# Kernel optimization log

Measured on AMD Instinct MI355X. Metric: run time of the kernel, lower is better.

Reference implementation:

```python
import jax, jax.numpy as jnp
import numpy as np

B, N, DI, DS, DP, DM, S = 64, 4096, 64, 64, 64, 128, 7
NUM_ITER = 3
EPS_ATTN = 1e-8
LN_EPS = 1e-5


def setup_inputs() -> dict:
    key = jax.random.key(0)
    ks = jax.random.split(key, 12)
    rn = lambda k, shp, sc=1.0: (jax.random.normal(k, shp, jnp.float32) * sc)
    return {
        "x": rn(ks[0], (B, N, DI)),
        "ln_inp_g": jnp.ones((DI,), jnp.float32),
        "ln_inp_b": jnp.zeros((DI,), jnp.float32),
        "ln_slot_g": jnp.ones((DS,), jnp.float32),
        "ln_slot_b": jnp.zeros((DS,), jnp.float32),
        "slots_init": rn(ks[1], (1, S, DS)),
        "Wk": rn(ks[2], (DI, DP), 1.0 / np.sqrt(DI)),
        "Wv": rn(ks[3], (DI, DP), 1.0 / np.sqrt(DI)),
        "Wq": rn(ks[4], (DS, DP), 1.0 / np.sqrt(DS)),
        "gru_wih": rn(ks[5], (3 * DS, DP), 1.0 / np.sqrt(DS)),
        "gru_whh": rn(ks[6], (3 * DS, DS), 1.0 / np.sqrt(DS)),
        "gru_bih": jnp.zeros((3 * DS,), jnp.float32),
        "gru_bhh": jnp.zeros((3 * DS,), jnp.float32),
        "mlp_w1": rn(ks[7], (DS, DM), 1.0 / np.sqrt(DS)),
        "mlp_b1": jnp.zeros((DM,), jnp.float32),
        "mlp_w2": rn(ks[8], (DM, DS), 1.0 / np.sqrt(DM)),
        "mlp_b2": jnp.zeros((DS,), jnp.float32),
    }


def _layernorm(x, g, b):
    m = jnp.mean(x, axis=-1, keepdims=True)
    v = jnp.mean(jnp.square(x - m), axis=-1, keepdims=True)
    return (x - m) * jax.lax.rsqrt(v + LN_EPS) * g + b


def _gru_cell(u, h, wih, whh, bih, bhh):
    # PyTorch GRUCell semantics
    gi = u @ wih.T + bih  # [*, 3*DS]
    gh = h @ whh.T + bhh
    ir, iz, inn = jnp.split(gi, 3, axis=-1)
    hr, hz, hn = jnp.split(gh, 3, axis=-1)
    r = jax.nn.sigmoid(ir + hr)
    z = jax.nn.sigmoid(iz + hz)
    n = jnp.tanh(inn + r * hn)
    return (1.0 - z) * n + z * h


def reference(x, ln_inp_g, ln_inp_b, ln_slot_g, ln_slot_b, slots_init,
              Wk, Wv, Wq, gru_wih, gru_whh, gru_bih, gru_bhh,
              mlp_w1, mlp_b1, mlp_w2, mlp_b2):
    x = _layernorm(x, ln_inp_g, ln_inp_b)          # [B,N,DI]
    k = x @ Wk                                      # [B,N,DP] (hoisted; x fixed across iters)
    v = x @ Wv                                      # [B,N,DP]
    slots = jnp.broadcast_to(slots_init, (x.shape[0], S, DS))
    scale = 1.0 / np.sqrt(DP)
    for _ in range(NUM_ITER):
        slots_prev = slots
        sn = _layernorm(slots, ln_slot_g, ln_slot_b)
        q = sn @ Wq                                 # [B,S,DP]
        attn = jnp.einsum('bnd,bsd->bns', k, q) * scale
        attn = jax.nn.softmax(attn, axis=-1) + EPS_ATTN      # softmax over slots
        weights = attn / jnp.sum(attn, axis=1, keepdims=True)  # normalize over N
        updates = jnp.einsum('bns,bnd->bsd', weights, v)     # [B,S,DP]
        h = _gru_cell(updates.reshape(-1, DP), slots_prev.reshape(-1, DS),
                      gru_wih, gru_whh, gru_bih, gru_bhh)
        slots = h.reshape(-1, S, DS)
        slots = slots + (jax.nn.relu(slots @ mlp_w1 + mlp_b1) @ mlp_w2 + mlp_b2)
    return slots
```

## Files before the change

### kernel.cpp

```cpp
#include <hip/hip_runtime.h>
#include <stdint.h>

#define L2E 1.44269504088896f

static __device__ __forceinline__ float wsum(float v) {
    #pragma unroll
    for (int m = 1; m < 64; m <<= 1) v += __shfl_xor(v, m, 64);
    return v;
}
static __device__ __forceinline__ float sigm(float x) {
    return 1.0f / (1.0f + __builtin_amdgcn_exp2f(-x * L2E));
}
static __device__ __forceinline__ float tanh_(float x) {
    const float ax = fabsf(x);
    const float t = __builtin_amdgcn_exp2f(-2.0f * ax * L2E);
    const float r = (1.0f - t) / (1.0f + t);
    return (x < 0.f) ? -r : r;
}

__global__ __launch_bounds__(256) void init_kernel(
    const float* __restrict__ s0,
    const float* __restrict__ lsg, const float* __restrict__ lsb,
    const float* __restrict__ Wq,  const float* __restrict__ Wk,
    const float* __restrict__ lig, const float* __restrict__ lib,
    const float* __restrict__ wih, const float* __restrict__ whh,
    float* __restrict__ slots, float* __restrict__ gkq, float* __restrict__ aux,
    float* __restrict__ wihT, float* __restrict__ whhT, float* __restrict__ WkT)
{
    __shared__ float wkT[4096];
    __shared__ float scr[4][64];
    const int tid = threadIdx.x, lane = tid & 63, wv = tid >> 6;
    const int idx = blockIdx.x * 256 + tid;

    if (idx < 12288) {
        const int i = idx / 192, j = idx - i * 192;
        wihT[idx] = wih[j * 64 + i];
    } else if (idx < 24576) {
        const int o = idx - 12288;
        const int i = o / 192, j = o - i * 192;
        whhT[o] = whh[j * 64 + i];
    } else {
        const int o = idx - 24576;
        const int p = o >> 6, d = o & 63;
        WkT[o] = Wk[d * 64 + p];
    }

    const int r = blockIdx.x * 4 + wv;
    const int s = r % 7;
    #pragma unroll
    for (int i = tid; i < 4096; i += 256) {
        const int d = i >> 6, p = i & 63;
        wkT[p * 64 + d] = Wk[i];
    }
    const float h = s0[s * 64 + lane];
    slots[r * 64 + lane] = h;
    __syncthreads();

    const float mean = wsum(h) * (1.0f / 64.0f);
    const float d = h - mean;
    const float var = wsum(d * d) * (1.0f / 64.0f);
    const float rs = rsqrtf(var + 1e-5f);
    const float sn = d * rs * lsg[lane] + lsb[lane];
    scr[wv][lane] = sn;
    __syncthreads();
    float q = 0.f;
    #pragma unroll 8
    for (int i = 0; i < 64; ++i) q = fmaf(scr[wv][i], Wq[i * 64 + lane], q);
    q *= 0.125f;
    __syncthreads();
    scr[wv][lane] = q;
    __syncthreads();
    float kq = 0.f;
    #pragma unroll 8
    for (int p = 0; p < 64; ++p) kq = fmaf(wkT[p * 64 + lane], scr[wv][p], kq);
    const float bk = wsum(lib[lane] * kq);
    const float gk = lig[lane] * kq;
    const float g1 = wsum(gk);
    gkq[r * 64 + lane] = gk;
    if (lane == 0) { aux[r * 2] = g1; aux[r * 2 + 1] = bk; }
}

__global__ __launch_bounds__(256) void attn_kernel(
    const float* __restrict__ x,
    const float* __restrict__ gkq, const float* __restrict__ aux,
    float* __restrict__ Ypart)
{
    __shared__ float xsh[4][32 * 65];
    __shared__ float wsh[4][32][8];
    __shared__ float gkql[448];
    __shared__ float auxl[14];
    __shared__ float ybuf[4][456];
    const int tid = threadIdx.x, lane = tid & 63, wv = tid >> 6;
    const int b = blockIdx.x >> 4, chunk = blockIdx.x & 15;

    gkql[tid] = gkq[b * 448 + tid];
    if (tid < 192) gkql[tid + 256] = gkq[b * 448 + tid + 256];
    if (tid < 14) auxl[tid] = aux[b * 14 + tid];
    __syncthreads();

    const int q5 = lane & 31, h = lane >> 5;
    float Yr[14];
    #pragma unroll
    for (int i = 0; i < 14; ++i) Yr[i] = 0.f;
    float cacc[7] = {0.f, 0.f, 0.f, 0.f, 0.f, 0.f, 0.f};

    const float* tbase = x + (((long)b * 4096) + chunk * 256 + wv * 64) * 64;
    #pragma unroll 1
    for (int pass = 0; pass < 2; ++pass) {
        const float4* src = (const float4*)(tbase + pass * 2048);
        #pragma unroll
        for (int st = 0; st < 8; ++st) {
            const float4 d4 = src[st * 64 + lane];
            const int f = (st * 64 + lane) * 4;
            const int row = f >> 6, dim = f & 63;
            float* dst = &xsh[wv][row * 65 + dim];
            dst[0] = d4.x; dst[1] = d4.y; dst[2] = d4.z; dst[3] = d4.w;
        }

        float xf[32];
        float sum = 0.f, ss = 0.f;
        const float* xr = &xsh[wv][q5 * 65 + h * 32];
        #pragma unroll
        for (int c = 0; c < 32; ++c) {
            xf[c] = xr[c];
            sum += xf[c];
            ss = fmaf(xf[c], xf[c], ss);
        }
        float acc[7];
        #pragma unroll
        for (int s = 0; s < 7; ++s) {
            float a = 0.f;
            const float* gk = &gkql[s * 64 + h * 32];
            #pragma unroll
            for (int c = 0; c < 32; ++c) a = fmaf(xf[c], gk[c], a);
            acc[s] = a;
        }
        sum += __shfl_xor(sum, 32, 64);
        ss  += __shfl_xor(ss, 32, 64);
        #pragma unroll
        for (int s = 0; s < 7; ++s) acc[s] += __shfl_xor(acc[s], 32, 64);

        const float m   = sum * (1.0f / 64.0f);
        const float var = ss * (1.0f / 64.0f) - m * m;
        const float rs  = rsqrtf(var + 1e-5f);
        const float rsm = rs * m;
        float t[7];
        #pragma unroll
        for (int s = 0; s < 7; ++s)
            t[s] = fmaf(rs, acc[s], fmaf(-rsm, auxl[2 * s], auxl[2 * s + 1]));
        float mx = t[0];
        #pragma unroll
        for (int s = 1; s < 7; ++s) mx = fmaxf(mx, t[s]);
        float e[7], se = 0.f;
        #pragma unroll
        for (int s = 0; s < 7; ++s) {
            e[s] = __builtin_amdgcn_exp2f((t[s] - mx) * L2E);
            se += e[s];
        }
        const float inv = 1.0f / se;
        #pragma unroll
        for (int s = 0; s < 7; ++s) {
            const float w = fmaf(e[s], inv, 1e-8f);
            cacc[s] += w;
            if (h == 0) wsh[wv][q5][s] = w * rs;
        }
        if (h == 0) wsh[wv][q5][7] = 0.f;

        #pragma unroll 4
        for (int r2 = 0; r2 < 16; ++r2) {
            const int rr = r2 * 2 + h;
            const float4 p0 = *(const float4*)&wsh[wv][rr][0];
            const float4 p1 = *(const float4*)&wsh[wv][rr][4];
            const float v0 = xsh[wv][rr * 65 + q5 * 2];
            const float v1 = xsh[wv][rr * 65 + q5 * 2 + 1];
            const float ps[7] = {p0.x, p0.y, p0.z, p0.w, p1.x, p1.y, p1.z};
            #pragma unroll
            for (int s = 0; s < 7; ++s) {
                Yr[2 * s]     = fmaf(ps[s], v0, Yr[2 * s]);
                Yr[2 * s + 1] = fmaf(ps[s], v1, Yr[2 * s + 1]);
            }
        }
    }

    #pragma unroll
    for (int i = 0; i < 14; ++i) Yr[i] += __shfl_xor(Yr[i], 32, 64);
    if (h == 0) {
        #pragma unroll
        for (int s = 0; s < 7; ++s) {
            ybuf[wv][s * 64 + q5 * 2]     = Yr[2 * s];
            ybuf[wv][s * 64 + q5 * 2 + 1] = Yr[2 * s + 1];
        }
    }
    #pragma unroll
    for (int s = 0; s < 7; ++s) {
        const float Cs = wsum(cacc[s]) * 0.5f;
        if (lane == 0) ybuf[wv][448 + s] = Cs;
    }
    if (lane == 1) ybuf[wv][455] = 0.f;
    __syncthreads();
    for (int i = tid; i < 455; i += 256)
        Ypart[((long)b * 16 + chunk) * 456 + i] =
            ybuf[0][i] + ybuf[1][i] + ybuf[2][i] + ybuf[3][i];
}

__global__ __launch_bounds__(256) void update_kernel(
    const float* __restrict__ Ypart, float* __restrict__ slots,
    const float* __restrict__ Wv,
    const float* __restrict__ wihT, const float* __restrict__ whhT,
    const float* __restrict__ bih,  const float* __restrict__ bhh,
    const float* __restrict__ w1,   const float* __restrict__ b1,
    const float* __restrict__ w2,   const float* __restrict__ b2,
    const float* __restrict__ lsg,  const float* __restrict__ lsb,
    const float* __restrict__ Wq,   const float* __restrict__ WkT,
    const float* __restrict__ lig,  const float* __restrict__ lib,
    float* __restrict__ gkq, float* __restrict__ aux,
    float* __restrict__ out, int last)
{
    __shared__ float red[4][64];
    __shared__ float c16[16];
    __shared__ float ash[64];
    __shared__ float ush[64];
    __shared__ float hsh[64];
    __shared__ float gish[192], ghsh[192];
    __shared__ float hnsh[64];
    __shared__ float mbsh[128];
    __shared__ float qsh[64];
    const int tid = threadIdx.x, lane = tid & 63, wv = tid >> 6;
    const int r = blockIdx.x;
    const int b = r / 7, s = r - b * 7;
    const float* Yb = Ypart + (long)b * 16 * 456;

    float yp = 0.f;
    #pragma unroll
    for (int c = 0; c < 4; ++c)
        yp += Yb[(wv * 4 + c) * 456 + s * 64 + lane];
    red[wv][lane] = yp;
    if (tid < 16) c16[tid] = Yb[tid * 456 + 448 + s];
    if (tid >= 64 && tid < 128) hsh[tid - 64] = slots[r * 64 + (tid - 64)];
    __syncthreads();

    if (tid < 64) {
        const float Yd = red[0][lane] + red[1][lane] + red[2][lane] + red[3][lane];
        float C = 0.f;
        #pragma unroll
        for (int c = 0; c < 16; ++c) C += c16[c];
        const float Z = wsum(Yd) * (1.0f / 64.0f);
        ash[lane] = (lig[lane] * (Yd - Z) + lib[lane] * C) / C;
    }
    __syncthreads();

    float up = 0.f;
    #pragma unroll
    for (int i = 0; i < 16; ++i) {
        const int ii = wv * 16 + i;
        up = fmaf(ash[ii], Wv[ii * 64 + lane], up);
    }
    red[wv][lane] = up;
    __syncthreads();
    if (tid < 64) ush[lane] = red[0][lane] + red[1][lane] + red[2][lane] + red[3][lane];
    __syncthreads();

    if (tid < 192) {
        float a1 = bih[tid], a2 = bhh[tid];
        #pragma unroll 8
        for (int i = 0; i < 64; ++i) {
            a1 = fmaf(ush[i], wihT[i * 192 + tid], a1);
            a2 = fmaf(hsh[i], whhT[i * 192 + tid], a2);
        }
        gish[tid] = a1; ghsh[tid] = a2;
    }
    __syncthreads();
    if (tid < 64) {
        const float rr = sigm(gish[tid] + ghsh[tid]);
        const float zz = sigm(gish[64 + tid] + ghsh[64 + tid]);
        const float nn = tanh_(gish[128 + tid] + rr * ghsh[128 + tid]);
        hnsh[tid] = (1.f - zz) * nn + zz * hsh[tid];
    }
    __syncthreads();

    if (tid < 128) {
        float m = b1[tid];
        #pragma unroll 8
        for (int i = 0; i < 64; ++i) m = fmaf(hnsh[i], w1[i * 128 + tid], m);
        mbsh[tid] = fmaxf(m, 0.f);
    }
    __syncthreads();

    if (tid < 64) {
        float o = b2[tid];
        #pragma unroll 8
        for (int t = 0; t < 128; ++t) o = fmaf(mbsh[t], w2[t * 64 + tid], o);
        const float snv = hnsh[tid] + o;
        slots[r * 64 + tid] = snv;
        if (last) {
            out[r * 64 + tid] = snv;
        } else {
            const float mean = wsum(snv) * (1.0f / 64.0f);
            const float d = snv - mean;
            const float var = wsum(d * d) * (1.0f / 64.0f);
            const float rs = rsqrtf(var + 1e-5f);
            const float sn = d * rs * lsg[tid] + lsb[tid];
            ash[tid] = sn;
            float q = 0.f;
            #pragma unroll 8
            for (int i = 0; i < 64; ++i) q = fmaf(ash[i], Wq[i * 64 + tid], q);
            qsh[tid] = q * 0.125f;
            float kq = 0.f;
            #pragma unroll 8
            for (int p = 0; p < 64; ++p) kq = fmaf(WkT[p * 64 + tid], qsh[p], kq);
            const float bk = wsum(lib[tid] * kq);
            const float gk = lig[tid] * kq;
            const float g1 = wsum(gk);
            gkq[r * 64 + tid] = gk;
            if (tid == 0) { aux[r * 2] = g1; aux[r * 2 + 1] = bk; }
        }
    }
}

extern "C" void kernel_launch(void* const* d_in, const int* in_sizes, int n_in,
                              void* d_out, int out_size, void* d_ws, size_t ws_size,
                              hipStream_t stream)
{
    const float* x   = (const float*)d_in[0];
    const float* lig = (const float*)d_in[1];
    const float* lib = (const float*)d_in[2];
    const float* lsg = (const float*)d_in[3];
    const float* lsb = (const float*)d_in[4];
    const float* s0  = (const float*)d_in[5];
    const float* Wk  = (const float*)d_in[6];
    const float* Wv  = (const float*)d_in[7];
    const float* Wq  = (const float*)d_in[8];
    const float* wih = (const float*)d_in[9];
    const float* whh = (const float*)d_in[10];
    const float* bih = (const float*)d_in[11];
    const float* bhh = (const float*)d_in[12];
    const float* w1  = (const float*)d_in[13];
    const float* b1  = (const float*)d_in[14];
    const float* w2  = (const float*)d_in[15];
    const float* b2  = (const float*)d_in[16];

    float* f = (float*)d_ws;
    float* gkq   = f; f += 448 * 64;
    float* aux   = f; f += 448 * 2;
    float* slots = f; f += 448 * 64;
    float* Ypart = f; f += (long)64 * 16 * 456;
    float* wihT  = f; f += 64 * 192;
    float* whhT  = f; f += 64 * 192;
    float* WkT   = f; f += 64 * 64;

    init_kernel<<<112, 256, 0, stream>>>(s0, lsg, lsb, Wq, Wk, lig, lib,
                                         wih, whh, slots, gkq, aux,
                                         wihT, whhT, WkT);
    for (int it = 0; it < 3; ++it) {
        attn_kernel<<<1024, 256, 0, stream>>>(x, gkq, aux, Ypart);
        update_kernel<<<448, 256, 0, stream>>>(
            Ypart, slots, Wv, wihT, whhT, bih, bhh, w1, b1, w2, b2,
            lsg, lsb, Wq, WkT, lig, lib, gkq, aux,
            (float*)d_out, it == 2);
    }
}
```

Measured before the change: 235.9 us.

## Restructure attention kernel to register-resident rows with DPP reductions

Rewrites the attention kernel so each 8-lane group owns one row of x, with each lane holding 8 dims in registers. Row stats and dot products are reduced with DPP row operations instead of LDS staging and cross-half shuffles. The weighted-value accumulation is done directly in registers, and the next rows are prefetched one step ahead. This removes the LDS transpose buffers and most LDS traffic, at the cost of heavy register use (56 accumulators plus 56 gk values) and a final 16-way LDS reduction.

```diff
diff --git a/kernel.cpp b/kernel.cpp
--- a/kernel.cpp
+++ b/kernel.cpp
@@ -16,6 +16,18 @@
     const float t = __builtin_amdgcn_exp2f(-2.0f * ax * L2E);
     const float r = (1.0f - t) / (1.0f + t);
     return (x < 0.f) ? -r : r;
+}
+
+template <int CTRL>
+static __device__ __forceinline__ float dppterm(float v) {
+    return __int_as_float(__builtin_amdgcn_update_dpp(
+        0, __float_as_int(v), CTRL, 0xF, 0xF, true));
+}
+static __device__ __forceinline__ float red8(float v) {
+    v += dppterm<0xB1>(v);
+    v += dppterm<0x4E>(v);
+    v += dppterm<0x141>(v);
+    return v;
 }
 
 __global__ __launch_bounds__(256) void init_kernel(
@@ -80,65 +92,65 @@
     if (lane == 0) { aux[r * 2] = g1; aux[r * 2 + 1] = bk; }
 }
 
-__global__ __launch_bounds__(256) void attn_kernel(
+__global__ __launch_bounds__(256, 2) void attn_kernel(
     const float* __restrict__ x,
     const float* __restrict__ gkq, const float* __restrict__ aux,
     float* __restrict__ Ypart)
 {
-    __shared__ float xsh[4][32 * 65];
-    __shared__ float wsh[4][32][8];
-    __shared__ float gkql[448];
-    __shared__ float auxl[14];
-    __shared__ float ybuf[4][456];
+    __shared__ float ybuf[16][460];
     const int tid = threadIdx.x, lane = tid & 63, wv = tid >> 6;
-    const int b = blockIdx.x >> 4, chunk = blockIdx.x & 15;
-
-    gkql[tid] = gkq[b * 448 + tid];
-    if (tid < 192) gkql[tid + 256] = gkq[b * 448 + tid + 256];
-    if (tid < 14) auxl[tid] = aux[b * 14 + tid];
-    __syncthreads();
-
-    const int q5 = lane & 31, h = lane >> 5;
-    float Yr[14];
-    #pragma unroll
-    for (int i = 0; i < 14; ++i) Yr[i] = 0.f;
+    const int b = blockIdx.x >> 4, chunk16 = blockIdx.x & 15;
+    const int ck  = lane & 7;
+    const int rsl = lane >> 3;
+
+    float gk[7][8];
+    {
+        const float4* gp = (const float4*)(gkq + b * 448 + ck * 8);
+        #pragma unroll
+        for (int s = 0; s < 7; ++s) {
+            const float4 u0 = gp[s * 16], u1 = gp[s * 16 + 1];
+            gk[s][0] = u0.x; gk[s][1] = u0.y; gk[s][2] = u0.z; gk[s][3] = u0.w;
+            gk[s][4] = u1.x; gk[s][5] = u1.y; gk[s][6] = u1.z; gk[s][7] = u1.w;
+        }
+    }
+    const float* ab = aux + b * 14;
+    float g1[7], bk[7];
+    #pragma unroll
+    for (int s = 0; s < 7; ++s) { g1[s] = ab[2 * s]; bk[s] = ab[2 * s + 1]; }
+
+    float Yacc[7][8];
+    #pragma unroll
+    for (int s = 0; s < 7; ++s)
+        #pragma unroll
+        for (int j = 0; j < 8; ++j) Yacc[s][j] = 0.f;
     float cacc[7] = {0.f, 0.f, 0.f, 0.f, 0.f, 0.f, 0.f};
 
-    const float* tbase = x + (((long)b * 4096) + chunk * 256 + wv * 64) * 64;
+    const float* rb = x + (((long)b * 4096) + chunk16 * 256 + wv * 64 + rsl) * 64
+                        + ck * 8;
+    float4 a0 = *(const float4*)(rb);
+    float4 a1 = *(const float4*)(rb + 4);
     #pragma unroll 1
-    for (int pass = 0; pass < 2; ++pass) {
-        const float4* src = (const float4*)(tbase + pass * 2048);
-        #pragma unroll
-        for (int st = 0; st < 8; ++st) {
-            const float4 d4 = src[st * 64 + lane];
-            const int f = (st * 64 + lane) * 4;
-            const int row = f >> 6, dim = f & 63;
-            float* dst = &xsh[wv][row * 65 + dim];
-            dst[0] = d4.x; dst[1] = d4.y; dst[2] = d4.z; dst[3] = d4.w;
-        }
-
-        float xf[32];
+    for (int g = 0; g < 8; ++g) {
+        const int gn = (g < 7) ? g + 1 : 7;
+        const float4 b0 = *(const float4*)(rb + gn * 512);
+        const float4 b1 = *(const float4*)(rb + gn * 512 + 4);
+
+        const float xv[8] = {a0.x, a0.y, a0.z, a0.w, a1.x, a1.y, a1.z, a1.w};
         float sum = 0.f, ss = 0.f;
-        const float* xr = &xsh[wv][q5 * 65 + h * 32];
-        #pragma unroll
-        for (int c = 0; c < 32; ++c) {
-            xf[c] = xr[c];
-            sum += xf[c];
-            ss = fmaf(xf[c], xf[c], ss);
-        }
+        #pragma unroll
+        for (int j = 0; j < 8; ++j) { sum += xv[j]; ss = fmaf(xv[j], xv[j], ss); }
         float acc[7];
         #pragma unroll
         for (int s = 0; s < 7; ++s) {
             float a = 0.f;
-            const float* gk = &gkql[s * 64 + h * 32];
             #pragma unroll
-            for (int c = 0; c < 32; ++c) a = fmaf(xf[c], gk[c], a);
+            for (int j = 0; j < 8; ++j) a = fmaf(xv[j], gk[s][j], a);
             acc[s] = a;
         }
-        sum += __shfl_xor(sum, 32, 64);
-        ss  += __shfl_xor(ss, 32, 64);
-        #pragma unroll
-        for (int s = 0; s < 7; ++s) acc[s] += __shfl_xor(acc[s], 32, 64);
+        sum = red8(sum);
+        ss  = red8(ss);
+        #pragma unroll
+        for (int s = 0; s < 7; ++s) acc[s] = red8(acc[s]);
 
         const float m   = sum * (1.0f / 64.0f);
         const float var = ss * (1.0f / 64.0f) - m * m;
@@ -147,7 +159,7 @@
         float t[7];
         #pragma unroll
         for (int s = 0; s < 7; ++s)
-            t[s] = fmaf(rs, acc[s], fmaf(-rsm, auxl[2 * s], auxl[2 * s + 1]));
+            t[s] = fmaf(rs, acc[s], fmaf(-rsm, g1[s], bk[s]));
         float mx = t[0];
         #pragma unroll
         for (int s = 1; s < 7; ++s) mx = fmaxf(mx, t[s]);
@@ -162,45 +174,42 @@
         for (int s = 0; s < 7; ++s) {
             const float w = fmaf(e[s], inv, 1e-8f);
             cacc[s] += w;
-            if (h == 0) wsh[wv][q5][s] = w * rs;
-        }
-        if (h == 0) wsh[wv][q5][7] = 0.f;
-
-        #pragma unroll 4
-        for (int r2 = 0; r2 < 16; ++r2) {
-            const int rr = r2 * 2 + h;
-            const float4 p0 = *(const float4*)&wsh[wv][rr][0];
-            const float4 p1 = *(const float4*)&wsh[wv][rr][4];
-            const float v0 = xsh[wv][rr * 65 + q5 * 2];
-            const float v1 = xsh[wv][rr * 65 + q5 * 2 + 1];
-            const float ps[7] = {p0.x, p0.y, p0.z, p0.w, p1.x, p1.y, p1.z};
+            const float wrs = w * rs;
             #pragma unroll
-            for (int s = 0; s < 7; ++s) {
-                Yr[2 * s]     = fmaf(ps[s], v0, Yr[2 * s]);
-                Yr[2 * s + 1] = fmaf(ps[s], v1, Yr[2 * s + 1]);
-            }
-        }
-    }
-
-    #pragma unroll
-    for (int i = 0; i < 14; ++i) Yr[i] += __shfl_xor(Yr[i], 32, 64);
-    if (h == 0) {
-        #pragma unroll
-        for (int s = 0; s < 7; ++s) {
-            ybuf[wv][s * 64 + q5 * 2]     = Yr[2 * s];
-            ybuf[wv][s * 64 + q5 * 2 + 1] = Yr[2 * s + 1];
-        }
-    }
+            for (int j = 0; j < 8; ++j)
+                Yacc[s][j] = fmaf(wrs, xv[j], Yacc[s][j]);
+        }
+        a0 = b0; a1 = b1;
+    }
+
     #pragma unroll
     for (int s = 0; s < 7; ++s) {
-        const float Cs = wsum(cacc[s]) * 0.5f;
-        if (lane == 0) ybuf[wv][448 + s] = Cs;
-    }
-    if (lane == 1) ybuf[wv][455] = 0.f;
-    __syncthreads();
-    for (int i = tid; i < 455; i += 256)
-        Ypart[((long)b * 16 + chunk) * 456 + i] =
-            ybuf[0][i] + ybuf[1][i] + ybuf[2][i] + ybuf[3][i];
+        #pragma unroll
+        for (int j = 0; j < 8; ++j)
+            Yacc[s][j] += dppterm<0x128>(Yacc[s][j]);
+        cacc[s] += dppterm<0x128>(cacc[s]);
+    }
+    if (((lane >> 3) & 1) == 0) {
+        const int sub = lane >> 4;
+        float* yb = &ybuf[wv * 4 + sub][ck * 8];
+        #pragma unroll
+        for (int s = 0; s < 7; ++s) {
+            #pragma unroll
+            for (int j = 0; j < 8; ++j) yb[s * 64 + j] = Yacc[s][j];
+        }
+        if (ck == 0) {
+            #pragma unroll
+            for (int s = 0; s < 7; ++s)
+                ybuf[wv * 4 + sub][448 + s] = cacc[s];
+        }
+    }
+    __syncthreads();
+    for (int i = tid; i < 455; i += 256) {
+        float v = 0.f;
+        #pragma unroll
+        for (int p = 0; p < 16; ++p) v += ybuf[p][i];
+        Ypart[((long)b * 16 + chunk16) * 456 + i] = v;
+    }
 }
 
 __global__ __launch_bounds__(256) void update_kernel(
```

After: 227.8 us. -3.4%, faster.
